# Performance work log

Hardware: AMD Instinct MI355X
Metric: run time of the kernel (lower is better)

Reference implementation:

```python
import jax, jax.numpy as jnp
import numpy as np

N = 100000
E = 1600000
N_IN = 512
N_H = 128


def setup_inputs() -> dict:
    key = jax.random.key(0)
    ks = jax.random.split(key, 8)
    x = jax.random.normal(ks[0], (N, N_IN), dtype=jnp.float32)
    src = jax.random.randint(ks[1], (E,), 0, N, dtype=jnp.int32)
    dst = jax.random.randint(ks[2], (E,), 0, N, dtype=jnp.int32)
    perm = jax.random.permutation(ks[3], N).astype(jnp.int32)
    # GraphConv params (in_feats=512 -> out_feats=128), xavier-ish scale
    W = jax.random.normal(ks[4], (N_IN, N_H), dtype=jnp.float32) / np.sqrt(N_IN)
    b = jnp.zeros((N_H,), dtype=jnp.float32)
    alpha = jnp.full((N_H,), 0.25, dtype=jnp.float32)  # PReLU(n_h) init
    mlp_W = jax.random.normal(ks[5], (N_H, N_H), dtype=jnp.float32) / np.sqrt(N_H)
    mlp_b = jnp.zeros((N_H,), dtype=jnp.float32)
    return {"x": x, "src": src, "dst": dst, "perm": perm, "W": W, "b": b,
            "alpha": alpha, "mlp_W": mlp_W, "mlp_b": mlp_b, "batch_train": 0}


def _degree_norm(idx, n):
    deg = jax.ops.segment_sum(jnp.ones_like(idx, dtype=jnp.float32), idx, num_segments=n)
    return jnp.clip(deg, 1.0, None) ** -0.5  # [n]


def _gcn_layer(x, src, dst, W, b, alpha):
    n = x.shape[0]
    norm_out = _degree_norm(src, n)  # src-side out-degree norm
    norm_in = _degree_norm(dst, n)   # dst-side in-degree norm
    # in_feats > out_feats: apply weight first (DGL GraphConv ordering)
    h = x @ W                                  # [N, n_h]
    h = h * norm_out[:, None]
    agg = jax.ops.segment_sum(h[src], dst, num_segments=n)  # SpMM copy_u/sum
    agg = agg * norm_in[:, None] + b
    return jnp.where(agg >= 0, agg, alpha * agg)  # PReLU(n_h)


def reference(x, src, dst, perm, W, b, alpha, mlp_W, mlp_b, batch_train):
    z1 = _gcn_layer(x, src, dst, W, b, alpha)          # clean encoder
    z2 = _gcn_layer(x[perm], src, dst, W, b, alpha)    # corrupted encoder
    z1 = z1 @ mlp_W + mlp_b
    z2 = z2 @ mlp_W + mlp_b
    logit = jnp.concatenate((z1.sum(1), z2.sum(1)), axis=0)  # [2N]
    return logit
```

## Files before the change

### kernel.cpp

```cpp
#include <hip/hip_runtime.h>


typedef __bf16 bf16x8 __attribute__((ext_vector_type(8)));
typedef float f32x4 __attribute__((ext_vector_type(4)));

#define PAD 48
#define NBMAX 256
#define EPB 4096

__device__ inline unsigned short f2bf(float f) {
  unsigned u = __float_as_uint(f);
  u += 0x7fffu + ((u >> 16) & 1u);
  return (unsigned short)(u >> 16);
}
__device__ inline float2 bfpair(unsigned u) {
  float2 r;
  r.x = __uint_as_float(u << 16);
  r.y = __uint_as_float(u & 0xffff0000u);
  return r;
}

__global__ __launch_bounds__(256) void k_bin(const int* __restrict__ src,
                                             const int* __restrict__ dst,
                                             int* __restrict__ gCntD,
                                             int* __restrict__ gCntS,
                                             int* __restrict__ dstbin,
                                             unsigned short* __restrict__ srcbin,
                                             int E, int NB, int CAP) {
  __shared__ int2 stage[EPB];
  __shared__ int cntD[NBMAX], cntS[NBMAX], baseD[NBMAX], baseS[NBMAX];
  const int tid = threadIdx.x;
  const int e0 = blockIdx.x * EPB;
  const int nloc = min(EPB, E - e0);

  for (int b = tid; b < NB; b += 256) { cntD[b] = 0; cntS[b] = 0; }
  __syncthreads();

#pragma unroll
  for (int it = 0; it < EPB / 256; ++it) {
    int i = it * 256 + tid;
    if (i < nloc) {
      int s = src[e0 + i];
      int d = dst[e0 + i];
      stage[i] = make_int2(s, d);
      atomicAdd(&cntD[d >> 9], 1);
      atomicAdd(&cntS[s >> 9], 1);
    }
  }
  __syncthreads();

  for (int b = tid; b < NB; b += 256) {
    baseD[b] = atomicAdd(&gCntD[b], cntD[b]);
    baseS[b] = atomicAdd(&gCntS[b], cntS[b]);
    cntD[b] = 0;
    cntS[b] = 0;
  }
  __syncthreads();

#pragma unroll
  for (int it = 0; it < EPB / 256; ++it) {
    int i = it * 256 + tid;
    if (i < nloc) {
      int2 sd = stage[i];
      int s = sd.x, d = sd.y;
      int bd = d >> 9;
      int p = atomicAdd(&cntD[bd], 1) + baseD[bd];
      if (p < CAP) dstbin[(size_t)bd * CAP + p] = (s << 9) | (d & 511);
      int bs = s >> 9;
      int q = atomicAdd(&cntS[bs], 1) + baseS[bs];
      if (q < CAP) srcbin[(size_t)bs * CAP + q] = (unsigned short)(s & 511);
    }
  }
}

__global__ __launch_bounds__(256) void k_csr(const int* __restrict__ gCntD,
                                             const int* __restrict__ dstbin,
                                             int* __restrict__ col,
                                             int* __restrict__ deg_d,
                                             float* __restrict__ norm_i,
                                             int N, int CAP) {
  __shared__ int cnt[512];
  const int b = blockIdx.x;
  const int tid = threadIdx.x;
  cnt[tid] = 0;
  cnt[tid + 256] = 0;
  __syncthreads();
  int cb = gCntD[b];
  if (cb > CAP) cb = CAP;
  const int* bin = dstbin + (size_t)b * CAP;
  for (int i = tid; i < cb; i += 256) {
    int rec = bin[i];
    int d9 = rec & 511;
    int s = rec >> 9;
    int pos = atomicAdd(&cnt[d9], 1);
    if (pos < PAD) col[((size_t)b * 512 + d9) * PAD + pos] = s;
  }
  __syncthreads();
  for (int t = tid; t < 512; t += 256) {
    int i = b * 512 + t;
    if (i < N) {
      int c = cnt[t];
      deg_d[i] = (c > PAD) ? PAD : c;
      norm_i[i] = rsqrtf((float)((c < 1) ? 1 : c));
    }
  }
}

__global__ __launch_bounds__(256) void k_shist(const int* __restrict__ gCntS,
                                               const unsigned short* __restrict__ srcbin,
                                               const int* __restrict__ perm,
                                               float* __restrict__ norm_o,
                                               int* __restrict__ inv,
                                               int N, int CAP) {
  __shared__ int hist[512];
  const int b = blockIdx.x;
  const int tid = threadIdx.x;
  hist[tid] = 0;
  hist[tid + 256] = 0;
  __syncthreads();
  int cb = gCntS[b];
  if (cb > CAP) cb = CAP;
  const unsigned short* bin = srcbin + (size_t)b * CAP;
  for (int i = tid; i < cb; i += 256) {
    atomicAdd(&hist[bin[i]], 1);
  }
  __syncthreads();
  for (int t = tid; t < 512; t += 256) {
    int i = b * 512 + t;
    if (i < N) {
      int h = hist[t];
      norm_o[i] = rsqrtf((float)((h < 1) ? 1 : h));
      inv[perm[i]] = i;
    }
  }
}

__global__ __launch_bounds__(256) void k_fill_dev(const int* __restrict__ src,
                                                  const int* __restrict__ dst,
                                                  int* __restrict__ deg_s,
                                                  int* __restrict__ cnt,
                                                  int* __restrict__ col, int E) {
  int t = blockIdx.x * 256 + threadIdx.x;
  int e0 = t * 4;
  if (e0 >= E) return;
  int e1 = (e0 + 4 < E) ? e0 + 4 : E;
  for (int e = e0; e < e1; e++) {
    int s = src[e], d = dst[e];
    atomicAdd(&deg_s[s], 1);
    int pos = atomicAdd(&cnt[d], 1);
    if (pos < PAD) col[(size_t)d * PAD + pos] = s;
  }
}

__global__ __launch_bounds__(256) void k_finish_dev(const int* __restrict__ deg_s,
                                                    const int* __restrict__ cnt,
                                                    const int* __restrict__ perm,
                                                    float* __restrict__ norm_o,
                                                    float* __restrict__ norm_i,
                                                    int* __restrict__ deg_d,
                                                    int* __restrict__ inv, int N) {
  int i = blockIdx.x * 256 + threadIdx.x;
  if (i >= N) return;
  int a = deg_s[i]; if (a < 1) a = 1;
  int b = cnt[i];
  deg_d[i] = (b > PAD) ? PAD : b;
  if (b < 1) b = 1;
  norm_o[i] = rsqrtf((float)a);
  norm_i[i] = rsqrtf((float)b);
  inv[perm[i]] = i;
}

__global__ __launch_bounds__(256) void k_castw(const float* __restrict__ W,
                                               unsigned short* __restrict__ WT) {
  int i = blockIdx.x * 256 + threadIdx.x;
  int k = i >> 7;
  int n = i & 127;
  WT[n * 512 + k] = f2bf(W[i]);
}

#define AS_STRIDE 40
__global__ __launch_bounds__(256) void k_gemm(const float* __restrict__ X,
                                              const unsigned short* __restrict__ WT,
                                              const float* __restrict__ norm_o,
                                              const int* __restrict__ inv,
                                              unsigned short* __restrict__ HH, int M) {
  __shared__ __align__(16) unsigned short smem[8192];
  unsigned short* As = smem;
  unsigned short* Bs = smem + 64 * AS_STRIDE;

  const int tid = threadIdx.x;
  const int wave = tid >> 6;
  const int lane = tid & 63;
  const int m = lane & 15;
  const int quad = lane >> 4;
  const int block_row = blockIdx.x * 64;

  f32x4 acc[8];
#pragma unroll
  for (int t = 0; t < 8; t++) acc[t] = (f32x4){0.f, 0.f, 0.f, 0.f};

  for (int k0 = 0; k0 < 512; k0 += 32) {
#pragma unroll
    for (int it = 0; it < 2; it++) {
      int idx = tid + it * 256;
      int row = idx >> 3;
      int kc = (idx & 7) * 4;
      int gr = block_row + row;
      float4 v = make_float4(0.f, 0.f, 0.f, 0.f);
      if (gr < M) v = *(const float4*)(X + (size_t)gr * 512 + k0 + kc);
      ushort4 b;
      b.x = f2bf(v.x); b.y = f2bf(v.y); b.z = f2bf(v.z); b.w = f2bf(v.w);
      *(ushort4*)&As[row * AS_STRIDE + kc] = b;
    }
#pragma unroll
    for (int it = 0; it < 2; it++) {
      int idx = tid + it * 256;
      int n = idx >> 2;
      int kc = (idx & 3) * 8;
      *(int4*)&Bs[n * AS_STRIDE + kc] = *(const int4*)(WT + (size_t)n * 512 + k0 + kc);
    }
    __syncthreads();

    bf16x8 a = *(bf16x8*)&As[(wave * 16 + m) * AS_STRIDE + quad * 8];
#pragma unroll
    for (int t = 0; t < 8; t++) {
      bf16x8 b = *(bf16x8*)&Bs[(t * 16 + m) * AS_STRIDE + quad * 8];
      acc[t] = __builtin_amdgcn_mfma_f32_16x16x32_bf16(a, b, acc[t], 0, 0, 0);
    }
    __syncthreads();
  }

  float no1[4], no2[4];
#pragma unroll
  for (int r = 0; r < 4; r++) {
    int rr = block_row + wave * 16 + quad * 4 + r;
    no1[r] = 0.f;
    no2[r] = 0.f;
    if (rr < M) {
      no1[r] = norm_o[rr];
      no2[r] = norm_o[inv[rr]];
    }
  }

#pragma unroll
  for (int t = 0; t < 8; t++) {
    int c = t * 16 + m;
#pragma unroll
    for (int r = 0; r < 4; r++) {
      int row = wave * 16 + quad * 4 + r;
      smem[row * 128 + c] = f2bf(acc[t][r] * no1[r]);
    }
  }
  __syncthreads();
#pragma unroll
  for (int it = 0; it < 4; it++) {
    int idx = tid + it * 256;
    int row = idx >> 4;
    int c8 = (idx & 15) * 8;
    int gr = block_row + row;
    if (gr < M)
      *(int4*)(HH + (size_t)gr * 256 + c8) = *(int4*)&smem[row * 128 + c8];
  }
  __syncthreads();

#pragma unroll
  for (int t = 0; t < 8; t++) {
    int c = t * 16 + m;
#pragma unroll
    for (int r = 0; r < 4; r++) {
      int row = wave * 16 + quad * 4 + r;
      smem[row * 128 + c] = f2bf(acc[t][r] * no2[r]);
    }
  }
  __syncthreads();
#pragma unroll
  for (int it = 0; it < 4; it++) {
    int idx = tid + it * 256;
    int row = idx >> 4;
    int c8 = (idx & 15) * 8;
    int gr = block_row + row;
    if (gr < M) {
      int q = inv[gr];
      *(int4*)(HH + (size_t)q * 256 + 128 + c8) = *(int4*)&smem[row * 128 + c8];
    }
  }
}

__global__ __launch_bounds__(128) void k_wsum(const float* __restrict__ mlpW,
                                              const float* __restrict__ mlpb,
                                              float* __restrict__ wsum,
                                              float* __restrict__ bsum) {
  __shared__ float sb[128];
  int k = threadIdx.x;
  float s = 0.f;
  for (int j = 0; j < 128; j++) s += mlpW[k * 128 + j];
  wsum[k] = s;
  sb[k] = mlpb[k];
  __syncthreads();
  for (int off = 64; off > 0; off >>= 1) {
    if (k < off) sb[k] += sb[k + off];
    __syncthreads();
  }
  if (k == 0) bsum[0] = sb[0];
}

__global__ __launch_bounds__(256) void k_agg(const unsigned short* __restrict__ HH,
                                             const int* __restrict__ deg_d,
                                             const int* __restrict__ col,
                                             const float* __restrict__ norm_i,
                                             const float* __restrict__ bias,
                                             const float* __restrict__ alpha,
                                             const float* __restrict__ wsum,
                                             const float* __restrict__ bsum,
                                             float* __restrict__ out, int N) {
  int wave = (blockIdx.x * 256 + threadIdx.x) >> 6;
  int lane = threadIdx.x & 63;
  if (wave >= N) return;
  const int g = lane >> 4;
  const int sl = lane & 15;

  int cl = deg_d[wave];
  const int* cbase = col + (size_t)wave * PAD;

  float a1[8], a2[8];
#pragma unroll
  for (int i = 0; i < 8; i++) { a1[i] = 0.f; a2[i] = 0.f; }

  for (int j0 = 0; j0 < cl; j0 += 4) {
    int j = j0 + g;
    int je = (j < cl) ? j : cl - 1;
    int s = cbase[je];
    float mk = (j < cl) ? 1.f : 0.f;
    const unsigned short* rp = HH + (size_t)s * 256 + sl * 8;
    int4 r1 = *(const int4*)rp;
    int4 r2 = *(const int4*)(rp + 128);
    const unsigned* u1 = (const unsigned*)&r1;
    const unsigned* u2 = (const unsigned*)&r2;
#pragma unroll
    for (int q = 0; q < 4; q++) {
      float2 v1 = bfpair(u1[q]);
      float2 v2 = bfpair(u2[q]);
      a1[2 * q]     = fmaf(v1.x, mk, a1[2 * q]);
      a1[2 * q + 1] = fmaf(v1.y, mk, a1[2 * q + 1]);
      a2[2 * q]     = fmaf(v2.x, mk, a2[2 * q]);
      a2[2 * q + 1] = fmaf(v2.y, mk, a2[2 * q + 1]);
    }
  }

#pragma unroll
  for (int i = 0; i < 8; i++) {
    a1[i] += __shfl_xor(a1[i], 16);
    a1[i] += __shfl_xor(a1[i], 32);
    a2[i] += __shfl_xor(a2[i], 16);
    a2[i] += __shfl_xor(a2[i], 32);
  }

  float ni = norm_i[wave];
  float4 bb0 = ((const float4*)bias)[sl * 2];
  float4 bb1 = ((const float4*)bias)[sl * 2 + 1];
  float4 al0 = ((const float4*)alpha)[sl * 2];
  float4 al1 = ((const float4*)alpha)[sl * 2 + 1];
  float4 ws0 = ((const float4*)wsum)[sl * 2];
  float4 ws1 = ((const float4*)wsum)[sl * 2 + 1];
  float bs = bsum[0];
  float bb[8] = {bb0.x, bb0.y, bb0.z, bb0.w, bb1.x, bb1.y, bb1.z, bb1.w};
  float al[8] = {al0.x, al0.y, al0.z, al0.w, al1.x, al1.y, al1.z, al1.w};
  float wsv[8] = {ws0.x, ws0.y, ws0.z, ws0.w, ws1.x, ws1.y, ws1.z, ws1.w};

  float p1 = 0.f, p2 = 0.f;
#pragma unroll
  for (int i = 0; i < 8; i++) {
    float g1 = a1[i] * ni + bb[i];
    float g2 = a2[i] * ni + bb[i];
    g1 = (g1 >= 0.f) ? g1 : al[i] * g1;
    g2 = (g2 >= 0.f) ? g2 : al[i] * g2;
    p1 = fmaf(g1, wsv[i], p1);
    p2 = fmaf(g2, wsv[i], p2);
  }
#pragma unroll
  for (int off = 8; off > 0; off >>= 1) {
    p1 += __shfl_down(p1, off);
    p2 += __shfl_down(p2, off);
  }
  if (lane == 0) {
    out[wave] = p1 + bs;
    out[N + wave] = p2 + bs;
  }
}


extern "C" void kernel_launch(void* const* d_in, const int* in_sizes, int n_in,
                              void* d_out, int out_size, void* d_ws, size_t ws_size,
                              hipStream_t stream) {
  const float* x = (const float*)d_in[0];
  const int* src = (const int*)d_in[1];
  const int* dst = (const int*)d_in[2];
  const int* perm = (const int*)d_in[3];
  const float* W = (const float*)d_in[4];
  const float* bias = (const float*)d_in[5];
  const float* alpha = (const float*)d_in[6];
  const float* mlpW = (const float*)d_in[7];
  const float* mlpb = (const float*)d_in[8];

  const int E = in_sizes[1];
  const int N = in_sizes[3];
  float* out = (float*)d_out;

  char* ws = (char*)d_ws;
  size_t off = 0;
  auto alloc = [&](size_t bytes) -> void* {
    void* p = ws + off;
    off = (off + bytes + 255) & ~(size_t)255;
    return p;
  };

  unsigned short* HH = (unsigned short*)alloc((size_t)N * 256 * sizeof(unsigned short));
  int* col = (int*)alloc((size_t)N * PAD * sizeof(int));
  unsigned short* WT = (unsigned short*)alloc(512 * 128 * sizeof(unsigned short));
  float* norm_o = (float*)alloc((size_t)N * sizeof(float));
  float* norm_i = (float*)alloc((size_t)N * sizeof(float));
  int* inv = (int*)alloc((size_t)N * sizeof(int));
  int* deg_d = (int*)alloc((size_t)N * sizeof(int));
  float* wsum = (float*)alloc(512);
  float* bsum = (float*)alloc(256);
  size_t common = off;

  const int NB = (N + 511) >> 9;
  const int meanB = (NB > 0) ? E / NB : 0;
  const int CAP = ((meanB * 5) / 4 + 1023) & ~1023;

  size_t need_binned = common + (size_t)NB * CAP * sizeof(int) +
                       (size_t)NB * CAP * sizeof(unsigned short) +
                       2 * (size_t)NBMAX * sizeof(int) + 4096;
  bool binned = (NB <= NBMAX) && ((ws_size == 0) || (ws_size >= need_binned));

  const int nbN = (N + 255) / 256;
  const int nbE4 = ((E + 3) / 4 + 255) / 256;

  k_castw<<<512 * 128 / 256, 256, 0, stream>>>(W, WT);
  k_wsum<<<1, 128, 0, stream>>>(mlpW, mlpb, wsum, bsum);

  if (binned) {
    int* dstbin = (int*)alloc((size_t)NB * CAP * sizeof(int));
    unsigned short* srcbin = (unsigned short*)alloc((size_t)NB * CAP * sizeof(unsigned short));
    int* gCntD = (int*)alloc((size_t)NBMAX * sizeof(int));
    int* gCntS = (int*)alloc((size_t)NBMAX * sizeof(int));
    hipMemsetAsync(gCntD, 0, (size_t)NBMAX * sizeof(int), stream);
    hipMemsetAsync(gCntS, 0, (size_t)NBMAX * sizeof(int), stream);
    const int nbBin = (E + EPB - 1) / EPB;
    k_bin<<<nbBin, 256, 0, stream>>>(src, dst, gCntD, gCntS, dstbin, srcbin,
                                     E, NB, CAP);
    k_csr<<<NB, 256, 0, stream>>>(gCntD, dstbin, col, deg_d, norm_i, N, CAP);
    k_shist<<<NB, 256, 0, stream>>>(gCntS, srcbin, perm, norm_o, inv, N, CAP);
  } else {
    int* deg_s = (int*)alloc((size_t)N * sizeof(int));
    int* cnt = (int*)alloc((size_t)N * sizeof(int));
    hipMemsetAsync(deg_s, 0, (size_t)N * sizeof(int), stream);
    hipMemsetAsync(cnt, 0, (size_t)N * sizeof(int), stream);
    k_fill_dev<<<nbE4, 256, 0, stream>>>(src, dst, deg_s, cnt, col, E);
    k_finish_dev<<<nbN, 256, 0, stream>>>(deg_s, cnt, perm, norm_o, norm_i,
                                          deg_d, inv, N);
  }

  k_gemm<<<(N + 63) / 64, 256, 0, stream>>>(x, WT, norm_o, inv, HH, N);
  k_agg<<<(N + 3) / 4, 256, 0, stream>>>(HH, deg_d, col, norm_i,
                                         bias, alpha, wsum, bsum, out, N);
}
```

Baseline: 531.3 us.

## Load GEMM operands directly from global memory into MFMA registers, dropping LDS staging

The GEMM no longer stages X and W tiles through shared memory with barriers. Each lane now loads its own A fragment straight from global memory, converts it to bf16 in registers, and reads B fragments of the transposed weight directly from global or L2, all inside a fully unrolled K loop. This removes the LDS writes, LDS reads and barriers. In exchange every wave re-fetches the whole weight matrix from cache, and the A loads are strided per lane rather than coalesced.

Result: slower. 565.2 us (+6.4%).

```diff
diff --git a/kernel.cpp b/kernel.cpp
--- a/kernel.cpp
+++ b/kernel.cpp
@@ -178,15 +178,12 @@
   WT[n * 512 + k] = f2bf(W[i]);
 }
 
-#define AS_STRIDE 40
 __global__ __launch_bounds__(256) void k_gemm(const float* __restrict__ X,
                                               const unsigned short* __restrict__ WT,
                                               const float* __restrict__ norm_o,
                                               const int* __restrict__ inv,
                                               unsigned short* __restrict__ HH, int M) {
   __shared__ __align__(16) unsigned short smem[8192];
-  unsigned short* As = smem;
-  unsigned short* Bs = smem + 64 * AS_STRIDE;
 
   const int tid = threadIdx.x;
   const int wave = tid >> 6;
@@ -195,39 +192,28 @@
   const int quad = lane >> 4;
   const int block_row = blockIdx.x * 64;
 
+  const int arow = block_row + wave * 16 + m;
+  const float* xrow = X + (size_t)((arow < M) ? arow : 0) * 512 + quad * 8;
+  const unsigned short* wbase = WT + (size_t)m * 512 + quad * 8;
+
   f32x4 acc[8];
 #pragma unroll
   for (int t = 0; t < 8; t++) acc[t] = (f32x4){0.f, 0.f, 0.f, 0.f};
 
-  for (int k0 = 0; k0 < 512; k0 += 32) {
-#pragma unroll
-    for (int it = 0; it < 2; it++) {
-      int idx = tid + it * 256;
-      int row = idx >> 3;
-      int kc = (idx & 7) * 4;
-      int gr = block_row + row;
-      float4 v = make_float4(0.f, 0.f, 0.f, 0.f);
-      if (gr < M) v = *(const float4*)(X + (size_t)gr * 512 + k0 + kc);
-      ushort4 b;
-      b.x = f2bf(v.x); b.y = f2bf(v.y); b.z = f2bf(v.z); b.w = f2bf(v.w);
-      *(ushort4*)&As[row * AS_STRIDE + kc] = b;
-    }
-#pragma unroll
-    for (int it = 0; it < 2; it++) {
-      int idx = tid + it * 256;
-      int n = idx >> 2;
-      int kc = (idx & 3) * 8;
-      *(int4*)&Bs[n * AS_STRIDE + kc] = *(const int4*)(WT + (size_t)n * 512 + k0 + kc);
-    }
-    __syncthreads();
-
-    bf16x8 a = *(bf16x8*)&As[(wave * 16 + m) * AS_STRIDE + quad * 8];
+#pragma unroll
+  for (int ks = 0; ks < 16; ks++) {
+    float4 va0 = *(const float4*)(xrow + ks * 32);
+    float4 va1 = *(const float4*)(xrow + ks * 32 + 4);
+    union { bf16x8 v; unsigned short us[8]; } au;
+    au.us[0] = f2bf(va0.x); au.us[1] = f2bf(va0.y);
+    au.us[2] = f2bf(va0.z); au.us[3] = f2bf(va0.w);
+    au.us[4] = f2bf(va1.x); au.us[5] = f2bf(va1.y);
+    au.us[6] = f2bf(va1.z); au.us[7] = f2bf(va1.w);
 #pragma unroll
     for (int t = 0; t < 8; t++) {
-      bf16x8 b = *(bf16x8*)&Bs[(t * 16 + m) * AS_STRIDE + quad * 8];
-      acc[t] = __builtin_amdgcn_mfma_f32_16x16x32_bf16(a, b, acc[t], 0, 0, 0);
-    }
-    __syncthreads();
+      bf16x8 b = *(const bf16x8*)(wbase + (size_t)t * 16 * 512 + ks * 32);
+      acc[t] = __builtin_amdgcn_mfma_f32_16x16x32_bf16(au.v, b, acc[t], 0, 0, 0);
+    }
   }
 
   float no1[4], no2[4];
```
